# Optimization experiments

Hardware: AMD Instinct MI355X
Metric: run time of the kernel (lower is better)

## Reference

```python
import jax, jax.numpy as jnp
import numpy as np

B, C, H, W = 16, 128, 56, 56
K = 3
F = K * K          # number of deformation filters = kernel taps
OUT = 512
STRIDE = 1


def setup_inputs() -> dict:
    key = jax.random.key(0)
    k1, k2, k3, k4 = jax.random.split(key, 4)
    x = jax.random.normal(k1, (B, C, H, W), jnp.float32)
    # Deform2d 1x1 offset conv: weight [2F, C], bias [2F] initialized to kernel tap offsets
    w_off = jax.random.normal(k2, (2 * F, C), jnp.float32) * 0.01
    half = K // 2
    xs = [float(dx) for dy in range(-half, K - half) for dx in range(-half, K - half)]
    ys = [float(dy) for dy in range(-half, K - half) for dx in range(-half, K - half)]
    b_off = jnp.array(xs + ys, jnp.float32)  # all x offsets first, then all y offsets
    # final 1x1 conv: [OUT, F*C]
    w_conv = jax.random.normal(k3, (OUT, F * C), jnp.float32) * (1.0 / np.sqrt(F * C))
    b_conv = jax.random.normal(k4, (OUT,), jnp.float32) * 0.01
    return {"x": x, "w_off": w_off, "b_off": b_off, "w_conv": w_conv, "b_conv": b_conv}


def _bilinear_sample(img, gx, gy):
    # img: [C,H,W]; gx, gy: [H,W] normalized coords in [-1,1]
    # torch grid_sample defaults: bilinear, zeros padding, align_corners=False
    C_, H_, W_ = img.shape
    ix = ((gx + 1.0) * W_ - 1.0) * 0.5
    iy = ((gy + 1.0) * H_ - 1.0) * 0.5
    x0 = jnp.floor(ix)
    y0 = jnp.floor(iy)
    wx1 = ix - x0
    wx0 = 1.0 - wx1
    wy1 = iy - y0
    wy0 = 1.0 - wy1

    def gather(yy, xx):
        valid = ((xx >= 0) & (xx < W_) & (yy >= 0) & (yy < H_)).astype(img.dtype)
        xi = jnp.clip(xx, 0, W_ - 1).astype(jnp.int32)
        yi = jnp.clip(yy, 0, H_ - 1).astype(jnp.int32)
        return img[:, yi, xi] * valid[None]  # [C,H,W]

    return (gather(y0, x0) * (wy0 * wx0)[None]
            + gather(y0, x0 + 1.0) * (wy0 * wx1)[None]
            + gather(y0 + 1.0, x0) * (wy1 * wx0)[None]
            + gather(y0 + 1.0, x0 + 1.0) * (wy1 * wx1)[None])


def reference(x, w_off, b_off, w_conv, b_conv):
    Bv, Cv, Hv, Wv = x.shape
    scale = 2.0 / max(Hv, Wv)
    # Deform2d: 1x1 conv -> per-pixel offsets, scaled to normalized grid units
    deform = (jnp.einsum('bchw,dc->bdhw', x, w_off) + b_off[None, :, None, None]) * scale
    # matches torch view(B*F, 2, H, W): consecutive channel pairs per filter
    deform = deform.reshape(Bv, F, 2, Hv, Wv)
    # identity grid from affine_grid (align_corners=False)
    base_x = (2.0 * jnp.arange(Wv, dtype=x.dtype) + 1.0) / Wv - 1.0
    base_y = (2.0 * jnp.arange(Hv, dtype=x.dtype) + 1.0) / Hv - 1.0
    # grid is detached in the torch code -> no gradient to the offset conv
    gx = jax.lax.stop_gradient(base_x[None, None, None, :] + deform[:, :, 0])  # [B,F,H,W]
    gy = jax.lax.stop_gradient(base_y[None, None, :, None] + deform[:, :, 1])  # [B,F,H,W]
    sample_f = jax.vmap(_bilinear_sample, in_axes=(None, 0, 0))   # over F filters (input shared)
    sample_bf = jax.vmap(sample_f, in_axes=(0, 0, 0))             # over batch
    sampled = sample_bf(x, gx, gy)                                 # [B,F,C,H,W]
    sampled = sampled.reshape(Bv, F * Cv, Hv, Wv)[:, :, ::STRIDE, ::STRIDE]
    # final 1x1 conv
    return jnp.einsum('bchw,oc->bohw', sampled, w_conv) + b_conv[None, :, None, None]
```

## Files before the change

### kernel.cpp

```cpp
#include <hip/hip_runtime.h>
#include <stdint.h>
#include <stddef.h>

#define BN 16
#define CN 128
#define HN 56
#define WN 56
#define HWN 3136
#define FN 9
#define DN 18
#define ON 512
#define KN 1152
#define MN 50176

typedef __bf16 bf16x8 __attribute__((ext_vector_type(8)));
typedef float f32x4 __attribute__((ext_vector_type(4)));

__device__ __forceinline__ unsigned short f2bf(float f) {
  unsigned int u = __builtin_bit_cast(unsigned int, f);
  u += 0x7fffu + ((u >> 16) & 1u);
  return (unsigned short)(u >> 16);
}

__device__ __forceinline__ void gload_lds16(const void* g, void* l) {
  __builtin_amdgcn_global_load_lds(
      (const __attribute__((address_space(1))) unsigned int*)g,
      (__attribute__((address_space(3))) unsigned int*)l, 16, 0, 0);
}

__global__ void k_transpose(const float* __restrict__ x, unsigned short* __restrict__ xt) {
  __shared__ float tile[32][33];
  const int b = blockIdx.z;
  const int hw0 = blockIdx.x * 32;
  const int c0 = blockIdx.y * 32;
  const int tx = threadIdx.x & 31;
  const int ty = threadIdx.x >> 5;
  const float* xb = x + (size_t)b * CN * HWN;
  unsigned short* xtb = xt + (size_t)b * HWN * CN;
#pragma unroll
  for (int r = 0; r < 4; ++r)
    tile[ty + r * 8][tx] = xb[(size_t)(c0 + ty + r * 8) * HWN + hw0 + tx];
  __syncthreads();
#pragma unroll
  for (int r = 0; r < 4; ++r)
    xtb[(size_t)(hw0 + ty + r * 8) * CN + c0 + tx] = f2bf(tile[tx][ty + r * 8]);
}

__global__ void k_wconv(const float4* __restrict__ w, ushort4* __restrict__ wb) {
  const int i = blockIdx.x * 256 + threadIdx.x;
  float4 v = w[i];
  ushort4 o;
  o.x = f2bf(v.x); o.y = f2bf(v.y); o.z = f2bf(v.z); o.w = f2bf(v.w);
  wb[i] = o;
}

__global__ void k_offsets(const unsigned short* __restrict__ xt, const float* __restrict__ w_off,
                          const float* __restrict__ b_off, float2* __restrict__ ixy) {
  __shared__ float lwoff[DN * CN];
  __shared__ float lboff[DN];
  for (int i = threadIdx.x; i < DN * CN; i += 256) lwoff[i] = w_off[i];
  if (threadIdx.x < DN) lboff[threadIdx.x] = b_off[threadIdx.x];
  __syncthreads();

  const int m = blockIdx.x * 256 + threadIdx.x;
  const int b = m / HWN;
  const int hw = m - b * HWN;
  const int h = hw / WN;
  const int w = hw - h * WN;
  const unsigned short* xp = xt + (size_t)m * CN;
  float acc[DN];
#pragma unroll
  for (int d = 0; d < DN; ++d) acc[d] = lboff[d];
  for (int c = 0; c < CN; c += 8) {
    bf16x8 xv = *(const bf16x8*)(xp + c);
    float xf[8];
#pragma unroll
    for (int q = 0; q < 8; ++q) xf[q] = (float)xv[q];
#pragma unroll
    for (int d = 0; d < DN; ++d) {
      float4 w0 = *(const float4*)(lwoff + d * CN + c);
      float4 w1 = *(const float4*)(lwoff + d * CN + c + 4);
      acc[d] += xf[0] * w0.x + xf[1] * w0.y + xf[2] * w0.z + xf[3] * w0.w
              + xf[4] * w1.x + xf[5] * w1.y + xf[6] * w1.z + xf[7] * w1.w;
    }
  }
  const float scale = 2.0f / 56.0f;
  const float bx = (2.0f * w + 1.0f) / (float)WN - 1.0f;
  const float by = (2.0f * h + 1.0f) / (float)HN - 1.0f;
#pragma unroll
  for (int f = 0; f < FN; ++f) {
    float gx = bx + acc[2 * f] * scale;
    float gy = by + acc[2 * f + 1] * scale;
    float ixv = ((gx + 1.0f) * (float)WN - 1.0f) * 0.5f;
    float iyv = ((gy + 1.0f) * (float)HN - 1.0f) * 0.5f;
    ixy[(size_t)m * FN + f] = make_float2(ixv, iyv);
  }
}

__global__ void k_sample(const unsigned short* __restrict__ xt, const float2* __restrict__ ixy,
                         unsigned short* __restrict__ S) {
  const int g = blockIdx.x * 256 + threadIdx.x;
  const int cc = g & 7;
  const int mf = g >> 3;
  const int m = mf / FN;
  const int f = mf - m * FN;
  const int b = m / HWN;

  const float2 p = ixy[mf];
  const float ix = p.x, iy = p.y;
  const float x0f = floorf(ix), y0f = floorf(iy);
  const float wx1 = ix - x0f, wy1 = iy - y0f;
  const float wx0 = 1.0f - wx1, wy0 = 1.0f - wy1;
  const int x0 = (int)x0f, y0 = (int)y0f;
  const int x1 = x0 + 1, y1 = y0 + 1;
  const bool vx0 = (x0 >= 0) & (x0 < WN), vx1 = (x1 >= 0) & (x1 < WN);
  const bool vy0 = (y0 >= 0) & (y0 < HN), vy1 = (y1 >= 0) & (y1 < HN);
  const float w00 = wy0 * wx0 * ((vy0 & vx0) ? 1.0f : 0.0f);
  const float w01 = wy0 * wx1 * ((vy0 & vx1) ? 1.0f : 0.0f);
  const float w10 = wy1 * wx0 * ((vy1 & vx0) ? 1.0f : 0.0f);
  const float w11 = wy1 * wx1 * ((vy1 & vx1) ? 1.0f : 0.0f);
  const int x0c = min(max(x0, 0), WN - 1), x1c = min(max(x1, 0), WN - 1);
  const int y0c = min(max(y0, 0), HN - 1), y1c = min(max(y1, 0), HN - 1);

  const unsigned short* bp = xt + (size_t)b * HWN * CN + cc * 16;
  const bf16x8* p00 = (const bf16x8*)(bp + (size_t)(y0c * WN + x0c) * CN);
  const bf16x8* p01 = (const bf16x8*)(bp + (size_t)(y0c * WN + x1c) * CN);
  const bf16x8* p10 = (const bf16x8*)(bp + (size_t)(y1c * WN + x0c) * CN);
  const bf16x8* p11 = (const bf16x8*)(bp + (size_t)(y1c * WN + x1c) * CN);
  bf16x8 a0 = p00[0], a1 = p00[1];
  bf16x8 b0 = p01[0], b1 = p01[1];
  bf16x8 c0 = p10[0], c1 = p10[1];
  bf16x8 d0 = p11[0], d1 = p11[1];

  unsigned short ov[16];
#pragma unroll
  for (int q = 0; q < 8; ++q) {
    float lo = w00 * (float)a0[q] + w01 * (float)b0[q] + w10 * (float)c0[q] + w11 * (float)d0[q];
    float hi = w00 * (float)a1[q] + w01 * (float)b1[q] + w10 * (float)c1[q] + w11 * (float)d1[q];
    ov[q] = f2bf(lo);
    ov[q + 8] = f2bf(hi);
  }
  uint4* dst = (uint4*)(S + (size_t)m * KN + f * CN + cc * 16);
  dst[0] = *(const uint4*)(ov);
  dst[1] = *(const uint4*)(ov + 8);
}

#define VMCNT4 asm volatile("s_waitcnt vmcnt(4)" ::: "memory")
#define VMCNT0 asm volatile("s_waitcnt vmcnt(0)" ::: "memory")
#define SBAR   asm volatile("s_barrier" ::: "memory")

__global__ __launch_bounds__(512, 2) void k_gemm(const unsigned short* __restrict__ Wb,
                                                 const unsigned short* __restrict__ S,
                                                 const float* __restrict__ bias,
                                                 float* __restrict__ out) {
  __shared__ __align__(128) char smem[131072];
  const int tid = threadIdx.x;
  const int wave = tid >> 6;
  const int lane = tid & 63;
  const int quad = lane >> 4;
  const int r16 = lane & 15;
  const int wm = wave >> 2;
  const int wn = wave & 3;

  const int bid = blockIdx.x;
  const int wgid = (bid & 7) * 49 + (bid >> 3);
  const int o0 = (wgid & 1) * 256;
  const int p0 = (wgid >> 1) * 256;

  f32x4 acc[2][2][4][2];
#pragma unroll
  for (int a = 0; a < 2; ++a)
#pragma unroll
    for (int b = 0; b < 2; ++b)
#pragma unroll
      for (int c = 0; c < 4; ++c)
#pragma unroll
        for (int d = 0; d < 2; ++d) acc[a][b][c][d] = (f32x4){0.f, 0.f, 0.f, 0.f};

  const int row0 = tid >> 3;
  const int chunk0 = (tid & 7) ^ (row0 & 7);
  const unsigned short* gA0 = Wb + (size_t)(o0 + row0) * KN + chunk0 * 8;
  const unsigned short* gB0 = S + (size_t)(p0 + row0) * KN + chunk0 * 8;

#define STAGE_A(PAR, HALF, KT) do {                                              \
    const unsigned short* g_ = gA0 + (size_t)(HALF) * 128 * KN + (size_t)(KT) * 64; \
    char* d_ = smem + (PAR) * 32768 + (HALF) * 16384 + tid * 16;                 \
    gload_lds16(g_, d_);                                                         \
    gload_lds16(g_ + (size_t)64 * KN, d_ + 8192);                                \
  } while (0)
#define STAGE_B(PAR, HALF, KT) do {                                              \
    const unsigned short* g_ = gB0 + (size_t)(HALF) * 128 * KN + (size_t)(KT) * 64; \
    char* d_ = smem + 65536 + (PAR) * 32768 + (HALF) * 16384 + tid * 16;         \
    gload_lds16(g_, d_);                                                         \
    gload_lds16(g_ + (size_t)64 * KN, d_ + 8192);                                \
  } while (0)

  const int rsw = r16 & 7;
  const int ch0 = (quad ^ rsw) * 16;
  const int ch1 = ch0 ^ 64;
  const int a_row = (wm * 64 + r16) * 128;
  const int b_row = (wn * 32 + r16) * 128;

#define PHASE(PAR, QI, QJ, STAGE_STMT, WAIT_STMT) do {                           \
    const char* pa_ = smem + (PAR) * 32768 + (QI) * 16384 + a_row;               \
    const char* pb_ = smem + 65536 + (PAR) * 32768 + (QJ) * 16384 + b_row;       \
    bf16x8 a0_ = *(const bf16x8*)(pa_ + 0 * 2048 + ch0);                         \
    bf16x8 a1_ = *(const bf16x8*)(pa_ + 1 * 2048 + ch0);                         \
    bf16x8 a2_ = *(const bf16x8*)(pa_ + 2 * 2048 + ch0);                         \
    bf16x8 a3_ = *(const bf16x8*)(pa_ + 3 * 2048 + ch0);                         \
    bf16x8 b0_ = *(const bf16x8*)(pb_ + 0 * 2048 + ch0);                         \
    bf16x8 b1_ = *(const bf16x8*)(pb_ + 1 * 2048 + ch0);                         \
    bf16x8 a4_ = *(const bf16x8*)(pa_ + 0 * 2048 + ch1);                         \
    bf16x8 a5_ = *(const bf16x8*)(pa_ + 1 * 2048 + ch1);                         \
    bf16x8 a6_ = *(const bf16x8*)(pa_ + 2 * 2048 + ch1);                         \
    bf16x8 a7_ = *(const bf16x8*)(pa_ + 3 * 2048 + ch1);                         \
    bf16x8 b2_ = *(const bf16x8*)(pb_ + 0 * 2048 + ch1);                         \
    bf16x8 b3_ = *(const bf16x8*)(pb_ + 1 * 2048 + ch1);                         \
    STAGE_STMT;                                                                  \
    WAIT_STMT;                                                                   \
    SBAR;                                                                        \
    __builtin_amdgcn_s_setprio(1);                                               \
    acc[QI][QJ][0][0] = __builtin_amdgcn_mfma_f32_16x16x32_bf16(a0_, b0_, acc[QI][QJ][0][0], 0, 0, 0); \
    acc[QI][QJ][0][1] = __builtin_amdgcn_mfma_f32_16x16x32_bf16(a0_, b1_, acc[QI][QJ][0][1], 0, 0, 0); \
    acc[QI][QJ][1][0] = __builtin_amdgcn_mfma_f32_16x16x32_bf16(a1_, b0_, acc[QI][QJ][1][0], 0, 0, 0); \
    acc[QI][QJ][1][1] = __builtin_amdgcn_mfma_f32_16x16x32_bf16(a1_, b1_, acc[QI][QJ][1][1], 0, 0, 0); \
    acc[QI][QJ][2][0] = __builtin_amdgcn_mfma_f32_16x16x32_bf16(a2_, b0_, acc[QI][QJ][2][0], 0, 0, 0); \
    acc[QI][QJ][2][1] = __builtin_amdgcn_mfma_f32_16x16x32_bf16(a2_, b1_, acc[QI][QJ][2][1], 0, 0, 0); \
    acc[QI][QJ][3][0] = __builtin_amdgcn_mfma_f32_16x16x32_bf16(a3_, b0_, acc[QI][QJ][3][0], 0, 0, 0); \
    acc[QI][QJ][3][1] = __builtin_amdgcn_mfma_f32_16x16x32_bf16(a3_, b1_, acc[QI][QJ][3][1], 0, 0, 0); \
    acc[QI][QJ][0][0] = __builtin_amdgcn_mfma_f32_16x16x32_bf16(a4_, b2_, acc[QI][QJ][0][0], 0, 0, 0); \
    acc[QI][QJ][0][1] = __builtin_amdgcn_mfma_f32_16x16x32_bf16(a4_, b3_, acc[QI][QJ][0][1], 0, 0, 0); \
    acc[QI][QJ][1][0] = __builtin_amdgcn_mfma_f32_16x16x32_bf16(a5_, b2_, acc[QI][QJ][1][0], 0, 0, 0); \
    acc[QI][QJ][1][1] = __builtin_amdgcn_mfma_f32_16x16x32_bf16(a5_, b3_, acc[QI][QJ][1][1], 0, 0, 0); \
    acc[QI][QJ][2][0] = __builtin_amdgcn_mfma_f32_16x16x32_bf16(a6_, b2_, acc[QI][QJ][2][0], 0, 0, 0); \
    acc[QI][QJ][2][1] = __builtin_amdgcn_mfma_f32_16x16x32_bf16(a6_, b3_, acc[QI][QJ][2][1], 0, 0, 0); \
    acc[QI][QJ][3][0] = __builtin_amdgcn_mfma_f32_16x16x32_bf16(a7_, b2_, acc[QI][QJ][3][0], 0, 0, 0); \
    acc[QI][QJ][3][1] = __builtin_amdgcn_mfma_f32_16x16x32_bf16(a7_, b3_, acc[QI][QJ][3][1], 0, 0, 0); \
    __builtin_amdgcn_s_setprio(0);                                               \
    SBAR;                                                                        \
  } while (0)

  STAGE_A(0, 0, 0); STAGE_B(0, 0, 0); STAGE_A(0, 1, 0); STAGE_B(0, 1, 0);
  STAGE_A(1, 0, 1); STAGE_B(1, 0, 1);
  VMCNT4;
  SBAR;

#pragma unroll 1
  for (int it = 0; it < 8; ++it) {
    const int t1 = 2 * it + 1, t2 = 2 * it + 2, t3 = 2 * it + 3;
    PHASE(0, 0, 0, STAGE_A(1, 1, t1), (void)0);
    PHASE(0, 0, 1, STAGE_B(1, 1, t1), (void)0);
    PHASE(0, 1, 0, STAGE_A(0, 0, t2), (void)0);
    PHASE(0, 1, 1, STAGE_B(0, 0, t2), VMCNT4);
    PHASE(1, 0, 0, STAGE_A(0, 1, t2), (void)0);
    PHASE(1, 0, 1, STAGE_B(0, 1, t2), (void)0);
    PHASE(1, 1, 0, STAGE_A(1, 0, t3), (void)0);
    PHASE(1, 1, 1, STAGE_B(1, 0, t3), VMCNT4);
  }
  PHASE(0, 0, 0, STAGE_A(1, 1, 17), (void)0);
  PHASE(0, 0, 1, STAGE_B(1, 1, 17), (void)0);
  PHASE(0, 1, 0, (void)0, (void)0);
  PHASE(0, 1, 1, (void)0, VMCNT0);
  PHASE(1, 0, 0, (void)0, (void)0);
  PHASE(1, 0, 1, (void)0, (void)0);
  PHASE(1, 1, 0, (void)0, (void)0);
  PHASE(1, 1, 1, (void)0, (void)0);

  float* lout = (float*)smem;
  const int LSTR = 260;
#pragma unroll
  for (int ob = 0; ob < 8; ++ob) {
    const int Qi = ob >> 2, wsel = (ob >> 1) & 1, s2 = ob & 1;
    __syncthreads();
    if (wm == wsel) {
#pragma unroll
      for (int il = 0; il < 2; ++il) {
        const int i = s2 * 2 + il;
#pragma unroll
        for (int Qj = 0; Qj < 2; ++Qj)
#pragma unroll
          for (int j = 0; j < 2; ++j) {
            f32x4 v = acc[Qi][Qj][i][j];
            const int col = Qj * 128 + wn * 32 + j * 16 + r16;
            const int rb = il * 16 + quad * 4;
            lout[(rb + 0) * LSTR + col] = v[0];
            lout[(rb + 1) * LSTR + col] = v[1];
            lout[(rb + 2) * LSTR + col] = v[2];
            lout[(rb + 3) * LSTR + col] = v[3];
          }
      }
    }
    __syncthreads();
#pragma unroll
    for (int tl = 0; tl < 4; ++tl) {
      const int idx = tl * 512 + tid;
      const int rr = idx >> 6, c4 = idx & 63;
      float4 v = *(const float4*)(lout + rr * LSTR + c4 * 4);
      const int o = o0 + ob * 32 + rr;
      const float bv = bias[o];
      v.x += bv; v.y += bv; v.z += bv; v.w += bv;
      const int p = p0 + c4 * 4;
      const int bidx = p / HWN;
      const int hw = p - bidx * HWN;
      *(float4*)(out + (size_t)bidx * ON * HWN + (size_t)o * HWN + hw) = v;
    }
  }
#undef PHASE
#undef STAGE_A
#undef STAGE_B
}

extern "C" void kernel_launch(void* const* d_in, const int* in_sizes, int n_in,
                              void* d_out, int out_size, void* d_ws, size_t ws_size,
                              hipStream_t stream) {
  const float* x = (const float*)d_in[0];
  const float* w_off = (const float*)d_in[1];
  const float* b_off = (const float*)d_in[2];
  const float* w_conv = (const float*)d_in[3];
  const float* b_conv = (const float*)d_in[4];
  float* out = (float*)d_out;

  char* ws = (char*)d_ws;
  unsigned short* xt = (unsigned short*)(ws);
  unsigned short* S = (unsigned short*)(ws + 12845056);
  unsigned short* Wb = (unsigned short*)(ws + 128450560);
  float2* ixy = (float2*)(ws + 129630208);

  k_transpose<<<dim3(98, 4, 16), 256, 0, stream>>>(x, xt);
  k_wconv<<<dim3(576), 256, 0, stream>>>((const float4*)w_conv, (ushort4*)Wb);
  k_offsets<<<dim3(196), 256, 0, stream>>>(xt, w_off, b_off, ixy);
  k_sample<<<dim3(14112), 256, 0, stream>>>(xt, ixy, S);
  k_gemm<<<dim3(392), 512, 0, stream>>>(Wb, S, b_conv, out);
}
```

Baseline: 251.2 us.

## Reuse LDS fragments across GEMM phases with snake quadrant order and reordered staging

The GEMM main loop now keeps A and B fragments in registers across the four quadrant phases. It visits quadrants in the order 00, 01, 11, 10, so each phase reloads only one operand from LDS (or none), where before every phase reloaded both. The global-to-LDS staging order is rearranged to match, the prologue stages one more B half, and the wait count rises from vmcnt(4) to vmcnt(6) to keep more loads in flight. The aim is fewer LDS reads per MFMA, at the cost of more live VGPRs for the fragments, which risks spills or lower occupancy at 512 threads with 2 blocks per CU.

```diff
diff --git a/kernel.cpp b/kernel.cpp
--- a/kernel.cpp
+++ b/kernel.cpp
@@ -145,7 +145,7 @@
   dst[1] = *(const uint4*)(ov + 8);
 }
 
-#define VMCNT4 asm volatile("s_waitcnt vmcnt(4)" ::: "memory")
+#define VMCNT6 asm volatile("s_waitcnt vmcnt(6)" ::: "memory")
 #define VMCNT0 asm volatile("s_waitcnt vmcnt(0)" ::: "memory")
 #define SBAR   asm volatile("s_barrier" ::: "memory")
 
@@ -201,70 +201,61 @@
   const int a_row = (wm * 64 + r16) * 128;
   const int b_row = (wn * 32 + r16) * 128;
 
-#define PHASE(PAR, QI, QJ, STAGE_STMT, WAIT_STMT) do {                           \
-    const char* pa_ = smem + (PAR) * 32768 + (QI) * 16384 + a_row;               \
-    const char* pb_ = smem + 65536 + (PAR) * 32768 + (QJ) * 16384 + b_row;       \
-    bf16x8 a0_ = *(const bf16x8*)(pa_ + 0 * 2048 + ch0);                         \
-    bf16x8 a1_ = *(const bf16x8*)(pa_ + 1 * 2048 + ch0);                         \
-    bf16x8 a2_ = *(const bf16x8*)(pa_ + 2 * 2048 + ch0);                         \
-    bf16x8 a3_ = *(const bf16x8*)(pa_ + 3 * 2048 + ch0);                         \
-    bf16x8 b0_ = *(const bf16x8*)(pb_ + 0 * 2048 + ch0);                         \
-    bf16x8 b1_ = *(const bf16x8*)(pb_ + 1 * 2048 + ch0);                         \
-    bf16x8 a4_ = *(const bf16x8*)(pa_ + 0 * 2048 + ch1);                         \
-    bf16x8 a5_ = *(const bf16x8*)(pa_ + 1 * 2048 + ch1);                         \
-    bf16x8 a6_ = *(const bf16x8*)(pa_ + 2 * 2048 + ch1);                         \
-    bf16x8 a7_ = *(const bf16x8*)(pa_ + 3 * 2048 + ch1);                         \
-    bf16x8 b2_ = *(const bf16x8*)(pb_ + 0 * 2048 + ch1);                         \
-    bf16x8 b3_ = *(const bf16x8*)(pb_ + 1 * 2048 + ch1);                         \
-    STAGE_STMT;                                                                  \
-    WAIT_STMT;                                                                   \
-    SBAR;                                                                        \
+  bf16x8 afr[8], bfr0[4], bfr1[4];
+
+#define LOAD_A(PAR, H) do {                                                      \
+    const char* pa_ = smem + (PAR) * 32768 + (H) * 16384 + a_row;                \
+    _Pragma("unroll") for (int i_ = 0; i_ < 4; ++i_) {                           \
+      afr[i_ * 2 + 0] = *(const bf16x8*)(pa_ + i_ * 2048 + ch0);                 \
+      afr[i_ * 2 + 1] = *(const bf16x8*)(pa_ + i_ * 2048 + ch1);                 \
+    } } while (0)
+#define LOAD_B(PAR, H, DST) do {                                                 \
+    const char* pb_ = smem + 65536 + (PAR) * 32768 + (H) * 16384 + b_row;        \
+    _Pragma("unroll") for (int j_ = 0; j_ < 2; ++j_) {                           \
+      DST[j_ * 2 + 0] = *(const bf16x8*)(pb_ + j_ * 2048 + ch0);                 \
+      DST[j_ * 2 + 1] = *(const bf16x8*)(pb_ + j_ * 2048 + ch1);                 \
+    } } while (0)
+#define MFMA16(QI, QJ, BF) do {                                                  \
     __builtin_amdgcn_s_setprio(1);                                               \
-    acc[QI][QJ][0][0] = __builtin_amdgcn_mfma_f32_16x16x32_bf16(a0_, b0_, acc[QI][QJ][0][0], 0, 0, 0); \
-    acc[QI][QJ][0][1] = __builtin_amdgcn_mfma_f32_16x16x32_bf16(a0_, b1_, acc[QI][QJ][0][1], 0, 0, 0); \
-    acc[QI][QJ][1][0] = __builtin_amdgcn_mfma_f32_16x16x32_bf16(a1_, b0_, acc[QI][QJ][1][0], 0, 0, 0); \
-    acc[QI][QJ][1][1] = __builtin_amdgcn_mfma_f32_16x16x32_bf16(a1_, b1_, acc[QI][QJ][1][1], 0, 0, 0); \
-    acc[QI][QJ][2][0] = __builtin_amdgcn_mfma_f32_16x16x32_bf16(a2_, b0_, acc[QI][QJ][2][0], 0, 0, 0); \
-    acc[QI][QJ][2][1] = __builtin_amdgcn_mfma_f32_16x16x32_bf16(a2_, b1_, acc[QI][QJ][2][1], 0, 0, 0); \
-    acc[QI][QJ][3][0] = __builtin_amdgcn_mfma_f32_16x16x32_bf16(a3_, b0_, acc[QI][QJ][3][0], 0, 0, 0); \
-    acc[QI][QJ][3][1] = __builtin_amdgcn_mfma_f32_16x16x32_bf16(a3_, b1_, acc[QI][QJ][3][1], 0, 0, 0); \
-    acc[QI][QJ][0][0] = __builtin_amdgcn_mfma_f32_16x16x32_bf16(a4_, b2_, acc[QI][QJ][0][0], 0, 0, 0); \
-    acc[QI][QJ][0][1] = __builtin_amdgcn_mfma_f32_16x16x32_bf16(a4_, b3_, acc[QI][QJ][0][1], 0, 0, 0); \
-    acc[QI][QJ][1][0] = __builtin_amdgcn_mfma_f32_16x16x32_bf16(a5_, b2_, acc[QI][QJ][1][0], 0, 0, 0); \
-    acc[QI][QJ][1][1] = __builtin_amdgcn_mfma_f32_16x16x32_bf16(a5_, b3_, acc[QI][QJ][1][1], 0, 0, 0); \
-    acc[QI][QJ][2][0] = __builtin_amdgcn_mfma_f32_16x16x32_bf16(a6_, b2_, acc[QI][QJ][2][0], 0, 0, 0); \
-    acc[QI][QJ][2][1] = __builtin_amdgcn_mfma_f32_16x16x32_bf16(a6_, b3_, acc[QI][QJ][2][1], 0, 0, 0); \
-    acc[QI][QJ][3][0] = __builtin_amdgcn_mfma_f32_16x16x32_bf16(a7_, b2_, acc[QI][QJ][3][0], 0, 0, 0); \
-    acc[QI][QJ][3][1] = __builtin_amdgcn_mfma_f32_16x16x32_bf16(a7_, b3_, acc[QI][QJ][3][1], 0, 0, 0); \
-    __builtin_amdgcn_s_setprio(0);                                               \
-    SBAR;                                                                        \
-  } while (0)
-
-  STAGE_A(0, 0, 0); STAGE_B(0, 0, 0); STAGE_A(0, 1, 0); STAGE_B(0, 1, 0);
-  STAGE_A(1, 0, 1); STAGE_B(1, 0, 1);
-  VMCNT4;
+    _Pragma("unroll") for (int i_ = 0; i_ < 4; ++i_)                             \
+    _Pragma("unroll") for (int j_ = 0; j_ < 2; ++j_) {                           \
+      acc[QI][QJ][i_][j_] = __builtin_amdgcn_mfma_f32_16x16x32_bf16(             \
+          afr[i_ * 2 + 0], BF[j_ * 2 + 0], acc[QI][QJ][i_][j_], 0, 0, 0);        \
+      acc[QI][QJ][i_][j_] = __builtin_amdgcn_mfma_f32_16x16x32_bf16(             \
+          afr[i_ * 2 + 1], BF[j_ * 2 + 1], acc[QI][QJ][i_][j_], 0, 0, 0);        \
+    }                                                                            \
+    __builtin_amdgcn_s_setprio(0); } while (0)
+
+#define PH00(PAR, STG, WT) do { LOAD_A(PAR, 0); LOAD_B(PAR, 0, bfr0); STG; WT; SBAR; MFMA16(0, 0, bfr0); SBAR; } while (0)
+#define PH01(PAR, STG, WT) do { LOAD_B(PAR, 1, bfr1); STG; WT; SBAR; MFMA16(0, 1, bfr1); SBAR; } while (0)
+#define PH11(PAR, STG, WT) do { LOAD_A(PAR, 1); STG; WT; SBAR; MFMA16(1, 1, bfr1); SBAR; } while (0)
+#define PH10(PAR, STG, WT) do { STG; WT; SBAR; MFMA16(1, 0, bfr0); SBAR; } while (0)
+
+  STAGE_A(0, 0, 0); STAGE_B(0, 0, 0); STAGE_B(0, 1, 0); STAGE_A(0, 1, 0);
+  STAGE_A(1, 0, 1); STAGE_B(1, 0, 1); STAGE_B(1, 1, 1);
+  VMCNT6;
   SBAR;
 
 #pragma unroll 1
   for (int it = 0; it < 8; ++it) {
     const int t1 = 2 * it + 1, t2 = 2 * it + 2, t3 = 2 * it + 3;
-    PHASE(0, 0, 0, STAGE_A(1, 1, t1), (void)0);
-    PHASE(0, 0, 1, STAGE_B(1, 1, t1), (void)0);
-    PHASE(0, 1, 0, STAGE_A(0, 0, t2), (void)0);
-    PHASE(0, 1, 1, STAGE_B(0, 0, t2), VMCNT4);
-    PHASE(1, 0, 0, STAGE_A(0, 1, t2), (void)0);
-    PHASE(1, 0, 1, STAGE_B(0, 1, t2), (void)0);
-    PHASE(1, 1, 0, STAGE_A(1, 0, t3), (void)0);
-    PHASE(1, 1, 1, STAGE_B(1, 0, t3), VMCNT4);
-  }
-  PHASE(0, 0, 0, STAGE_A(1, 1, 17), (void)0);
-  PHASE(0, 0, 1, STAGE_B(1, 1, 17), (void)0);
-  PHASE(0, 1, 0, (void)0, (void)0);
-  PHASE(0, 1, 1, (void)0, VMCNT0);
-  PHASE(1, 0, 0, (void)0, (void)0);
-  PHASE(1, 0, 1, (void)0, (void)0);
-  PHASE(1, 1, 0, (void)0, (void)0);
-  PHASE(1, 1, 1, (void)0, (void)0);
+    PH00(0, STAGE_A(1, 1, t1), (void)0);
+    PH01(0, STAGE_A(0, 0, t2), (void)0);
+    PH11(0, STAGE_B(0, 0, t2), (void)0);
+    PH10(0, STAGE_B(0, 1, t2), VMCNT6);
+    PH00(1, STAGE_A(0, 1, t2), (void)0);
+    PH01(1, STAGE_A(1, 0, t3), (void)0);
+    PH11(1, STAGE_B(1, 0, t3), (void)0);
+    PH10(1, STAGE_B(1, 1, t3), VMCNT6);
+  }
+  PH00(0, STAGE_A(1, 1, 17), (void)0);
+  PH01(0, (void)0, (void)0);
+  PH11(0, (void)0, (void)0);
+  PH10(0, (void)0, VMCNT0);
+  PH00(1, (void)0, (void)0);
+  PH01(1, (void)0, (void)0);
+  PH11(1, (void)0, (void)0);
+  PH10(1, (void)0, (void)0);
 
   float* lout = (float*)smem;
   const int LSTR = 260;
@@ -305,7 +296,13 @@
       *(float4*)(out + (size_t)bidx * ON * HWN + (size_t)o * HWN + hw) = v;
     }
   }
-#undef PHASE
+#undef PH00
+#undef PH01
+#undef PH11
+#undef PH10
+#undef MFMA16
+#undef LOAD_A
+#undef LOAD_B
 #undef STAGE_A
 #undef STAGE_B
 }
```

New measurement: 248.5 us. No clear change (-1.0%).
